# Kernel optimization log

Measured on AMD Instinct MI355X. Metric: run time of the kernel, lower is better.

## Reference

```python
import jax, jax.numpy as jnp
import numpy as np

D_MODEL = 4096
D_FIBER = 64
D_LATENT = 512
OMEGA = 0.1
B, L = 4, 4096


def cayley(A):
    # Q = (I - A)^{-1} (I + A), batched over leading dim; A is skew-symmetric
    d = A.shape[-1]
    I = jnp.eye(d, dtype=A.dtype)
    return jnp.linalg.solve(I - A, I + A)


def setup_inputs() -> dict:
    key = jax.random.key(0)
    k1, k2, k3, k4, k5 = jax.random.split(key, 5)
    h_t = jax.random.normal(k1, (B, L, D_MODEL), dtype=jnp.float32)
    z0 = jax.random.normal(k2, (B, D_LATENT), dtype=jnp.float32)
    A_raw = jax.random.normal(k3, (B, D_FIBER, D_FIBER), dtype=jnp.float32) * 0.1
    A_u = A_raw - jnp.swapaxes(A_raw, -1, -2)  # skew-symmetric gauge connection
    # frozen projection weights, torch nn.Linear layout: (out_features, in_features)
    W_down = jax.random.normal(k4, (D_FIBER, D_MODEL), dtype=jnp.float32) / np.sqrt(D_MODEL)
    W_up = jax.random.normal(k5, (D_MODEL, D_FIBER), dtype=jnp.float32) / np.sqrt(D_FIBER)
    alpha = jnp.float32(OMEGA)
    return {"h_t": h_t, "z0": z0, "A_u": A_u, "alpha": alpha, "W_down": W_down, "W_up": W_up}


def reference(h_t, z0, A_u, alpha, W_down, W_up):
    # psi_down: (B,L,d_model) @ (d_model,d_fiber)
    h_fiber = jnp.einsum('bld,fd->blf', h_t, W_down)
    Q_u = cayley(A_u)  # (B, d_fiber, d_fiber)
    # h_fiber @ Q_u^T per batch
    h_rot = jnp.einsum('blf,bgf->blg', h_fiber, Q_u)
    delta = h_rot - h_fiber
    h_out = h_t + alpha * jnp.einsum('blf,df->bld', delta, W_up)
    return h_out
```

## Files before the change

kernel.cpp:

```cpp
#include <hip/hip_runtime.h>
#include <hip/hip_bf16.h>

#define D_MODEL 4096
#define NFIB    64
#define NBATCH  4
#define LSEQ    4096
#define TM      32
#define NTILE   (LSEQ / TM)
#define KC      256
#define NCH     (D_MODEL / KC)

typedef __attribute__((ext_vector_type(4))) float f32x4;
typedef __attribute__((ext_vector_type(8))) short bf16x8;

__device__ __forceinline__ unsigned short f2bf(float f) {
  unsigned int u = __builtin_bit_cast(unsigned int, f);
  u += 0x7FFFu + ((u >> 16) & 1u);
  return (unsigned short)(u >> 16);
}

__device__ __forceinline__ bf16x8 cvt8(f32x4 a, f32x4 b) {
  union { __hip_bfloat162 h2[4]; bf16x8 v; } u;
  u.h2[0] = __float22bfloat162_rn(make_float2(a[0], a[1]));
  u.h2[1] = __float22bfloat162_rn(make_float2(a[2], a[3]));
  u.h2[2] = __float22bfloat162_rn(make_float2(b[0], b[1]));
  u.h2[3] = __float22bfloat162_rn(make_float2(b[2], b[3]));
  return u.v;
}

__global__ __launch_bounds__(256) void prep1_kernel(const float* __restrict__ A,
                                                    const float* __restrict__ Wd,
                                                    float* __restrict__ S,
                                                    unsigned short* __restrict__ Wd2) {
  const int blk = blockIdx.x;
  if (blk >= NBATCH) {
    int idx = (blk - NBATCH) * 256 + threadIdx.x;
    int j    = idx & 7;
    int lane = (idx >> 3) & 63;
    int nf   = (idx >> 9) & 3;
    int ks   = idx >> 11;
    int row = nf * 16 + (lane & 15);
    int col = ks * 32 + (lane >> 4) * 8 + j;
    Wd2[idx] = f2bf(Wd[row * D_MODEL + col]);
    return;
  }
  __shared__ float M[64][66];
  __shared__ float R[64][66];
  const int b = blk;
  const int tid = threadIdx.x;
  const int k = tid & 63;
  const int g = tid >> 6;
  const float* Ab = A + b * 4096;
#pragma unroll
  for (int ii = 0; ii < 16; ++ii) {
    int i = g * 16 + ii;
    float a = Ab[i * 64 + k];
    M[i][k] = ((i == k) ? 1.0f : 0.0f) - a;
    R[i][k] = 2.0f * a;
  }
  for (int j = 0; j < 64; ++j) {
    __syncthreads();
    float pr  = 1.0f / M[j][j];
    float mjk = M[j][k], rjk = R[j][k];
    float f[16];
#pragma unroll
    for (int ii = 0; ii < 16; ++ii) f[ii] = M[g * 16 + ii][j] * pr;
    __syncthreads();
#pragma unroll
    for (int ii = 0; ii < 16; ++ii) {
      int i = g * 16 + ii;
      if (i != j) { M[i][k] -= f[ii] * mjk; R[i][k] -= f[ii] * rjk; }
    }
  }
  __syncthreads();
  float* Sb = S + b * 4096;
#pragma unroll
  for (int ii = 0; ii < 16; ++ii) {
    int i = g * 16 + ii;
    Sb[i * 64 + k] = R[i][k] / M[i][i];
  }
}

__global__ __launch_bounds__(256) void prep_u_kernel(const float* __restrict__ Wup,
                                                     const float* __restrict__ S,
                                                     const float* __restrict__ alpha_p,
                                                     unsigned short* __restrict__ U2) {
  __shared__ float Sl[4096];
  const int idx0 = blockIdx.x * 256;
  const int b = idx0 >> 18;
  const float* Sb = S + b * 4096;
  for (int i = threadIdx.x; i < 1024; i += 256)
    ((f32x4*)Sl)[i] = ((const f32x4*)Sb)[i];
  __syncthreads();
  const int idx = idx0 + threadIdx.x;
  const int j    = idx & 7;
  const int h    = (idx >> 3) & 1;
  const int lane = (idx >> 4) & 63;
  const int nt   = (idx >> 10) & 255;
  const int d = nt * 16 + (lane & 15);
  const int f = h * 32 + (lane >> 4) * 8 + j;
  const float alpha = alpha_p[0];
  const f32x4* wr = (const f32x4*)(Wup + d * 64);
  float s = 0.f;
#pragma unroll
  for (int g4 = 0; g4 < 16; ++g4) {
    f32x4 wv = wr[g4];
    s += wv[0] * Sl[(g4 * 4 + 0) * 64 + f] + wv[1] * Sl[(g4 * 4 + 1) * 64 + f] +
         wv[2] * Sl[(g4 * 4 + 2) * 64 + f] + wv[3] * Sl[(g4 * 4 + 3) * 64 + f];
  }
  U2[idx] = f2bf(alpha * s);
}

__global__ __launch_bounds__(512, 4) void main_kernel(
    const float* __restrict__ H, const unsigned short* __restrict__ Wd2,
    const unsigned short* __restrict__ U2, float* __restrict__ Out) {
  const int blk = blockIdx.x;
  const int b = blk >> 7;
  const int t = blk & 127;
  const int row0 = b * LSEQ + t * TM;

  const int tid = threadIdx.x;
  const int w = tid >> 6, l = tid & 63, lr = l & 15, lq = l >> 4;
  const int wgT = w >> 2, wgF = w & 3;

  __shared__ float Hs[2 * TM * KC];
  __shared__ __attribute__((aligned(16))) unsigned short Fb[TM][72];

  const char* hb = (const char*)(H + (size_t)row0 * D_MODEL);
  auto lds3 = (__attribute__((address_space(3))) char*)Hs;

#define STAGE(KCH, BUF)                                                          \
  {                                                                              \
    _Pragma("unroll")                                                            \
    for (int q = 0; q < 4; ++q) {                                                \
      int i = (w << 2) + q;                                                      \
      const char* g = hb + (size_t)i * 16384 + (size_t)(KCH) * 1024 +            \
                      ((l * 16) ^ ((i & 7) << 4));                               \
      __builtin_amdgcn_global_load_lds(                                          \
          (const __attribute__((address_space(1))) void*)g,                      \
          (__attribute__((address_space(3))) void*)(lds3 + (BUF) * 32768 +       \
                                                    i * 1024),                   \
          16, 0, 0);                                                             \
    }                                                                            \
  }

  f32x4 acc = {0, 0, 0, 0};
  const int rowA = wgT * 16 + lr;
  const int abase = rowA * 1024;
  const int axor = (rowA & 7) << 4;

  STAGE(0, 0);
  for (int k = 0; k < NCH; ++k) {
    const int buf = k & 1;
    if (k + 1 < NCH) {
      STAGE(k + 1, buf ^ 1);
      asm volatile("s_waitcnt vmcnt(4)" ::: "memory");
    } else {
      asm volatile("s_waitcnt vmcnt(0)" ::: "memory");
    }
    __builtin_amdgcn_s_barrier();
    __builtin_amdgcn_sched_barrier(0);

#pragma unroll
    for (int s = 0; s < 8; ++s) {
      const int coff = s * 128 + lq * 32;
      f32x4 h0 = *(const f32x4*)((const char*)Hs + buf * 32768 + abase + ((coff) ^ axor));
      f32x4 h1 = *(const f32x4*)((const char*)Hs + buf * 32768 + abase + ((coff + 16) ^ axor));
      bf16x8 bfr = *(const bf16x8*)(Wd2 + (((size_t)(k * 8 + s) * 4 + wgF) * 64 + l) * 8);
      acc = __builtin_amdgcn_mfma_f32_16x16x32_bf16(cvt8(h0, h1), bfr, acc, 0, 0, 0);
    }
    __builtin_amdgcn_s_barrier();
  }
#undef STAGE

#pragma unroll
  for (int rr = 0; rr < 4; ++rr)
    Fb[wgT * 16 + lq * 4 + rr][wgF * 16 + lr] = f2bf(acc[rr]);
  __syncthreads();

  const int tg = w >> 2, dq = w & 3;
  bf16x8 fb0 = *(const bf16x8*)(&Fb[tg * 16 + lr][lq * 8]);
  bf16x8 fb1 = *(const bf16x8*)(&Fb[tg * 16 + lr][32 + lq * 8]);

  const unsigned short* ub = U2 + (((size_t)b * 256 + dq * 64) * 64 + l) * 16;
  const size_t obase = (size_t)(row0 + tg * 16 + lr) * D_MODEL + dq * 1024 + lq * 4;

  bf16x8 u0r[2], u1r[2];
  f32x4 hr[2];
#pragma unroll
  for (int q = 0; q < 2; ++q) {
    u0r[q] = *(const bf16x8*)(ub + q * 1024);
    u1r[q] = *(const bf16x8*)(ub + q * 1024 + 8);
    hr[q]  = *(const f32x4*)(H + obase + q * 16);
  }

#pragma unroll
  for (int nf = 0; nf < 64; ++nf) {
    f32x4 c = {0, 0, 0, 0};
    c = __builtin_amdgcn_mfma_f32_16x16x32_bf16(u0r[nf & 1], fb0, c, 0, 0, 0);
    c = __builtin_amdgcn_mfma_f32_16x16x32_bf16(u1r[nf & 1], fb1, c, 0, 0, 0);
    f32x4 r = hr[nf & 1];
    if (nf + 2 < 64) {
      u0r[nf & 1] = *(const bf16x8*)(ub + (nf + 2) * 1024);
      u1r[nf & 1] = *(const bf16x8*)(ub + (nf + 2) * 1024 + 8);
      hr[nf & 1]  = *(const f32x4*)(H + obase + (nf + 2) * 16);
    }
    *(f32x4*)(Out + obase + nf * 16) = r + c;
  }
}

extern "C" void kernel_launch(void* const* d_in, const int* in_sizes, int n_in,
                              void* d_out, int out_size, void* d_ws, size_t ws_size,
                              hipStream_t stream) {
  const float* h_t    = (const float*)d_in[0];
  const float* A_u    = (const float*)d_in[2];
  const float* alpha  = (const float*)d_in[3];
  const float* W_down = (const float*)d_in[4];
  const float* W_up   = (const float*)d_in[5];
  float* out = (float*)d_out;

  char* ws = (char*)d_ws;
  float*          S   = (float*)ws;
  unsigned short* Wd2 = (unsigned short*)(ws + 65536);
  unsigned short* U2  = (unsigned short*)(ws + 65536 + 524288);

  prep1_kernel<<<NBATCH + 1024, 256, 0, stream>>>(A_u, W_down, S, Wd2);
  prep_u_kernel<<<4096, 256, 0, stream>>>(W_up, S, alpha, U2);
  main_kernel<<<NBATCH * NTILE, 512, 0, stream>>>(h_t, Wd2, U2, out);
}
```

Baseline: 326.8 us.

## Split fused main kernel into down-projection and up-projection kernels for more parallelism

```diff
diff --git a/kernel.cpp b/kernel.cpp
--- a/kernel.cpp
+++ b/kernel.cpp
@@ -5,10 +5,6 @@
 #define NFIB    64
 #define NBATCH  4
 #define LSEQ    4096
-#define TM      32
-#define NTILE   (LSEQ / TM)
-#define KC      256
-#define NCH     (D_MODEL / KC)
 
 typedef __attribute__((ext_vector_type(4))) float f32x4;
 typedef __attribute__((ext_vector_type(8))) short bf16x8;
@@ -86,73 +82,78 @@
                                                      const float* __restrict__ alpha_p,
                                                      unsigned short* __restrict__ U2) {
   __shared__ float Sl[4096];
-  const int idx0 = blockIdx.x * 256;
-  const int b = idx0 >> 18;
+  const int blk = blockIdx.x;
+  const int b = blk >> 7;
+  const int ntg = blk & 127;
   const float* Sb = S + b * 4096;
   for (int i = threadIdx.x; i < 1024; i += 256)
     ((f32x4*)Sl)[i] = ((const f32x4*)Sb)[i];
   __syncthreads();
-  const int idx = idx0 + threadIdx.x;
-  const int j    = idx & 7;
-  const int h    = (idx >> 3) & 1;
-  const int lane = (idx >> 4) & 63;
-  const int nt   = (idx >> 10) & 255;
+
+  const int t = threadIdx.x;
+  const int nt   = ntg * 2 + (t >> 7);
+  const int h    = (t >> 6) & 1;
+  const int lane = t & 63;
   const int d = nt * 16 + (lane & 15);
-  const int f = h * 32 + (lane >> 4) * 8 + j;
+  const int fbase = h * 32 + (lane >> 4) * 8;
   const float alpha = alpha_p[0];
   const f32x4* wr = (const f32x4*)(Wup + d * 64);
-  float s = 0.f;
+
+  float s[8];
+#pragma unroll
+  for (int j = 0; j < 8; ++j) s[j] = 0.f;
 #pragma unroll
   for (int g4 = 0; g4 < 16; ++g4) {
     f32x4 wv = wr[g4];
-    s += wv[0] * Sl[(g4 * 4 + 0) * 64 + f] + wv[1] * Sl[(g4 * 4 + 1) * 64 + f] +
-         wv[2] * Sl[(g4 * 4 + 2) * 64 + f] + wv[3] * Sl[(g4 * 4 + 3) * 64 + f];
-  }
-  U2[idx] = f2bf(alpha * s);
-}
-
-__global__ __launch_bounds__(512, 4) void main_kernel(
+#pragma unroll
+    for (int gg = 0; gg < 4; ++gg) {
+      const float* srow = &Sl[(g4 * 4 + gg) * 64 + fbase];
+      float wvg = wv[gg];
+#pragma unroll
+      for (int j = 0; j < 8; ++j) s[j] += wvg * srow[j];
+    }
+  }
+  bf16x8 v;
+#pragma unroll
+  for (int j = 0; j < 8; ++j) v[j] = (short)f2bf(alpha * s[j]);
+  *(bf16x8*)(U2 + ((((size_t)b * 256 + nt) * 64 + lane) * 2 + h) * 8) = v;
+}
+
+__global__ __launch_bounds__(256, 4) void p1_kernel(
     const float* __restrict__ H, const unsigned short* __restrict__ Wd2,
-    const unsigned short* __restrict__ U2, float* __restrict__ Out) {
-  const int blk = blockIdx.x;
-  const int b = blk >> 7;
-  const int t = blk & 127;
-  const int row0 = b * LSEQ + t * TM;
-
+    unsigned short* __restrict__ F2) {
+  const int blk = blockIdx.x;
+  const int row0 = blk * 16;
   const int tid = threadIdx.x;
   const int w = tid >> 6, l = tid & 63, lr = l & 15, lq = l >> 4;
-  const int wgT = w >> 2, wgF = w & 3;
-
-  __shared__ float Hs[2 * TM * KC];
-  __shared__ __attribute__((aligned(16))) unsigned short Fb[TM][72];
-
+
+  __shared__ float Hs[2 * 16 * 256];
+  auto lds3 = (__attribute__((address_space(3))) char*)Hs;
   const char* hb = (const char*)(H + (size_t)row0 * D_MODEL);
-  auto lds3 = (__attribute__((address_space(3))) char*)Hs;
-
-#define STAGE(KCH, BUF)                                                          \
-  {                                                                              \
-    _Pragma("unroll")                                                            \
-    for (int q = 0; q < 4; ++q) {                                                \
-      int i = (w << 2) + q;                                                      \
-      const char* g = hb + (size_t)i * 16384 + (size_t)(KCH) * 1024 +            \
-                      ((l * 16) ^ ((i & 7) << 4));                               \
-      __builtin_amdgcn_global_load_lds(                                          \
-          (const __attribute__((address_space(1))) void*)g,                      \
-          (__attribute__((address_space(3))) void*)(lds3 + (BUF) * 32768 +       \
-                                                    i * 1024),                   \
-          16, 0, 0);                                                             \
-    }                                                                            \
+
+#define STAGE(KCH, BUF)                                                        \
+  {                                                                            \
+    _Pragma("unroll")                                                          \
+    for (int q = 0; q < 4; ++q) {                                              \
+      int i = w * 4 + q;                                                       \
+      const char* g = hb + (size_t)i * 16384 + (KCH) * 1024 +                  \
+                      ((l * 16) ^ ((i & 7) << 4));                             \
+      __builtin_amdgcn_global_load_lds(                                        \
+          (const __attribute__((address_space(1))) void*)g,                    \
+          (__attribute__((address_space(3))) void*)(lds3 + (BUF) * 16384 +     \
+                                                    i * 1024),                 \
+          16, 0, 0);                                                           \
+    }                                                                          \
   }
 
   f32x4 acc = {0, 0, 0, 0};
-  const int rowA = wgT * 16 + lr;
-  const int abase = rowA * 1024;
-  const int axor = (rowA & 7) << 4;
+  const int abase = lr * 1024;
+  const int axor = (lr & 7) << 4;
 
   STAGE(0, 0);
-  for (int k = 0; k < NCH; ++k) {
+  for (int k = 0; k < 16; ++k) {
     const int buf = k & 1;
-    if (k + 1 < NCH) {
+    if (k < 15) {
       STAGE(k + 1, buf ^ 1);
       asm volatile("s_waitcnt vmcnt(4)" ::: "memory");
     } else {
@@ -160,13 +161,12 @@
     }
     __builtin_amdgcn_s_barrier();
     __builtin_amdgcn_sched_barrier(0);
-
 #pragma unroll
     for (int s = 0; s < 8; ++s) {
       const int coff = s * 128 + lq * 32;
-      f32x4 h0 = *(const f32x4*)((const char*)Hs + buf * 32768 + abase + ((coff) ^ axor));
-      f32x4 h1 = *(const f32x4*)((const char*)Hs + buf * 32768 + abase + ((coff + 16) ^ axor));
-      bf16x8 bfr = *(const bf16x8*)(Wd2 + (((size_t)(k * 8 + s) * 4 + wgF) * 64 + l) * 8);
+      f32x4 h0 = *(const f32x4*)((const char*)Hs + buf * 16384 + abase + (coff ^ axor));
+      f32x4 h1 = *(const f32x4*)((const char*)Hs + buf * 16384 + abase + ((coff + 16) ^ axor));
+      bf16x8 bfr = *(const bf16x8*)(Wd2 + (((size_t)(k * 8 + s) * 4 + w) * 64 + l) * 8);
       acc = __builtin_amdgcn_mfma_f32_16x16x32_bf16(cvt8(h0, h1), bfr, acc, 0, 0, 0);
     }
     __builtin_amdgcn_s_barrier();
@@ -175,15 +175,28 @@
 
 #pragma unroll
   for (int rr = 0; rr < 4; ++rr)
-    Fb[wgT * 16 + lq * 4 + rr][wgF * 16 + lr] = f2bf(acc[rr]);
-  __syncthreads();
-
-  const int tg = w >> 2, dq = w & 3;
-  bf16x8 fb0 = *(const bf16x8*)(&Fb[tg * 16 + lr][lq * 8]);
-  bf16x8 fb1 = *(const bf16x8*)(&Fb[tg * 16 + lr][32 + lq * 8]);
-
-  const unsigned short* ub = U2 + (((size_t)b * 256 + dq * 64) * 64 + l) * 16;
-  const size_t obase = (size_t)(row0 + tg * 16 + lr) * D_MODEL + dq * 1024 + lq * 4;
+    F2[(size_t)(row0 + lq * 4 + rr) * 64 + w * 16 + lr] = f2bf(acc[rr]);
+}
+
+__global__ __launch_bounds__(256, 8) void p2_kernel(
+    const float* __restrict__ H, const unsigned short* __restrict__ F2,
+    const unsigned short* __restrict__ U2, float* __restrict__ Out) {
+  const int blk = blockIdx.x;
+  const int tile = blk >> 1;
+  const int ch = blk & 1;
+  const int row0 = tile * 16;
+  const int b = row0 >> 12;
+  const int tid = threadIdx.x;
+  const int w = tid >> 6, l = tid & 63, lr = l & 15, lq = l >> 4;
+
+  const int cbase = ch * 2048 + w * 512;
+  const int nt0 = cbase >> 4;
+
+  bf16x8 fb0 = *(const bf16x8*)(F2 + (size_t)(row0 + lr) * 64 + lq * 8);
+  bf16x8 fb1 = *(const bf16x8*)(F2 + (size_t)(row0 + lr) * 64 + 32 + lq * 8);
+
+  const unsigned short* ub = U2 + (((size_t)b * 256 + nt0) * 64 + l) * 16;
+  const size_t obase = (size_t)(row0 + lr) * D_MODEL + cbase + lq * 4;
 
   bf16x8 u0r[2], u1r[2];
   f32x4 hr[2];
@@ -195,12 +208,12 @@
   }
 
 #pragma unroll
-  for (int nf = 0; nf < 64; ++nf) {
+  for (int nf = 0; nf < 32; ++nf) {
     f32x4 c = {0, 0, 0, 0};
     c = __builtin_amdgcn_mfma_f32_16x16x32_bf16(u0r[nf & 1], fb0, c, 0, 0, 0);
     c = __builtin_amdgcn_mfma_f32_16x16x32_bf16(u1r[nf & 1], fb1, c, 0, 0, 0);
     f32x4 r = hr[nf & 1];
-    if (nf + 2 < 64) {
+    if (nf + 2 < 32) {
       u0r[nf & 1] = *(const bf16x8*)(ub + (nf + 2) * 1024);
       u1r[nf & 1] = *(const bf16x8*)(ub + (nf + 2) * 1024 + 8);
       hr[nf & 1]  = *(const f32x4*)(H + obase + (nf + 2) * 16);
@@ -221,10 +234,12 @@
 
   char* ws = (char*)d_ws;
   float*          S   = (float*)ws;
-  unsigned short* Wd2 = (unsigned short*)(ws + 65536);
-  unsigned short* U2  = (unsigned short*)(ws + 65536 + 524288);
+  unsigned short* Wd2 = (unsigned short*)(ws + (64 << 10));
+  unsigned short* U2  = (unsigned short*)(ws + (576 << 10));
+  unsigned short* F2  = (unsigned short*)(ws + (2624 << 10));
 
   prep1_kernel<<<NBATCH + 1024, 256, 0, stream>>>(A_u, W_down, S, Wd2);
-  prep_u_kernel<<<4096, 256, 0, stream>>>(W_up, S, alpha, U2);
-  main_kernel<<<NBATCH * NTILE, 512, 0, stream>>>(h_t, Wd2, U2, out);
-}
+  prep_u_kernel<<<512, 256, 0, stream>>>(W_up, S, alpha, U2);
+  p1_kernel<<<1024, 256, 0, stream>>>(h_t, Wd2, F2);
+  p2_kernel<<<2048, 256, 0, stream>>>(h_t, F2, U2, out);
+}
```

Result: faster. 311.8 us (-4.6%).
